# Optimization experiments

Hardware: AMD Instinct MI355X
Metric: run time of the kernel (lower is better)

Reference implementation:

```python
import jax, jax.numpy as jnp
import numpy as np

B, T, C = 2, 2048, 2048
HK, HV, DK, DV, KW = 16, 32, 128, 128, 4
KEY_DIM = HK * DK          # 2048
VAL_DIM = HV * DV          # 4096
QKV_DIM = 2 * KEY_DIM + VAL_DIM  # 8192
REPEAT = HV // HK
EPS = 1e-6


def setup_inputs() -> dict:
    key = jax.random.key(0)
    ks = jax.random.split(key, 12)
    s = 0.02
    return {
        "x": jax.random.normal(ks[0], (B, T, C), jnp.float32),
        "positions": jnp.arange(B * T, dtype=jnp.int64).reshape(B, T) % T,
        "W_qkv": jax.random.normal(ks[1], (QKV_DIM, C), jnp.float32) * s,
        "W_z": jax.random.normal(ks[2], (VAL_DIM, C), jnp.float32) * s,
        "W_b": jax.random.normal(ks[3], (HV, C), jnp.float32) * s,
        "W_a": jax.random.normal(ks[4], (HV, C), jnp.float32) * s,
        "conv_w": jax.random.normal(ks[5], (QKV_DIM, 1, KW), jnp.float32) * 0.3,
        "dt_bias": jnp.ones((HV,), jnp.float32),
        "A_log": jnp.log(jax.random.uniform(ks[6], (HV,), jnp.float32, 0.01, 16.0)),
        "norm_w": jnp.ones((DV,), jnp.float32),
        "W_out": jax.random.normal(ks[7], (C, VAL_DIM), jnp.float32) * s,
    }


def _forward(x, W_qkv, W_z, W_b, W_a, conv_w, dt_bias, A_log, norm_w, W_out):
    qkv = x @ W_qkv.T                                # [B,T,QKV_DIM]
    z = (x @ W_z.T).reshape(B, T, HV, DV)
    b = x @ W_b.T                                    # [B,T,HV]
    a = x @ W_a.T                                    # [B,T,HV]

    # depthwise causal conv1d (left pad KW-1), then SiLU
    qkv_c = jnp.transpose(qkv, (0, 2, 1))            # [B,QKV_DIM,T]
    qkv_c = jax.lax.conv_general_dilated(
        qkv_c, conv_w, window_strides=(1,), padding=[(KW - 1, 0)],
        dimension_numbers=("NCH", "OIH", "NCH"), feature_group_count=QKV_DIM)
    qkv = jax.nn.silu(jnp.transpose(qkv_c, (0, 2, 1)))

    q, k, v = jnp.split(qkv, [KEY_DIM, 2 * KEY_DIM], axis=-1)
    q = q.reshape(B, T, HK, DK)
    k = k.reshape(B, T, HK, DK)
    v = v.reshape(B, T, HV, DV)
    q = q / jnp.maximum(jnp.linalg.norm(q, axis=-1, keepdims=True), 1e-12)
    k = k / jnp.maximum(jnp.linalg.norm(k, axis=-1, keepdims=True), 1e-12)
    if REPEAT > 1:
        q = jnp.repeat(q, REPEAT, axis=2)            # [B,T,HV,DK]
        k = jnp.repeat(k, REPEAT, axis=2)

    beta = jax.nn.sigmoid(b)                         # [B,T,HV]
    g = -jnp.exp(A_log) * jax.nn.softplus(a + dt_bias)  # [B,T,HV]

    # gated delta-rule recurrence over time (lax.scan, time-major)
    def step(state, inp):
        g_t, beta_t, k_t, v_t, q_t = inp             # [B,HV], [B,HV], [B,HV,DK], [B,HV,DV], [B,HV,DK]
        state = jnp.exp(g_t)[..., None, None] * state \
            + beta_t[..., None, None] * (k_t[..., :, None] * v_t[..., None, :])
        out_t = jnp.einsum("bhk,bhkv->bhv", q_t, state)
        return state, out_t

    tm = lambda u: jnp.moveaxis(u, 1, 0)
    state0 = jnp.zeros((B, HV, DK, DV), x.dtype)
    _, out = jax.lax.scan(step, state0, (tm(g), tm(beta), tm(k), tm(v), tm(q)))
    out = jnp.moveaxis(out, 0, 1)                    # [B,T,HV,DV]

    # gated RMSNorm per head: RMSNorm(out) * silu(z)
    o = out.astype(jnp.float32)
    o = o * jax.lax.rsqrt(jnp.mean(o * o, axis=-1, keepdims=True) + EPS)
    o = (norm_w * o) * jax.nn.silu(z.astype(jnp.float32))
    o = o.astype(x.dtype).reshape(B, T, VAL_DIM)
    return o @ W_out.T                               # [B,T,C]


def reference(x, positions, W_qkv, W_z, W_b, W_a, conv_w, dt_bias, A_log, norm_w, W_out):
    del positions  # unused by the module's math
    return _forward(x, W_qkv, W_z, W_b, W_a, conv_w, dt_bias, A_log, norm_w, W_out)
```

## Files before the change

kernel.cpp:

```cpp
#include <hip/hip_runtime.h>

typedef unsigned short u16;
typedef unsigned int u32;
typedef __attribute__((ext_vector_type(8))) short short8;
typedef __attribute__((ext_vector_type(8))) _Float16 half8;
typedef __attribute__((ext_vector_type(4))) float f32x4;

#define NB 2
#define NT 2048
#define NC 2048
#define NHV 32
#define VALD 4096
#define NBT 4096
#define CL 64
#define NCH (NT / CL)

#define GL16(gp, lp) __builtin_amdgcn_global_load_lds( \
    (const __attribute__((address_space(1))) unsigned int*)(gp), \
    (__attribute__((address_space(3))) unsigned int*)(lp), 16, 0, 0)

static __device__ __forceinline__ float bf2f(u16 u) {
  union { u32 u; float f; } x; x.u = ((u32)u) << 16; return x.f;
}
static __device__ __forceinline__ u16 f2bf(float f) {
  union { float f; u32 u; } x; x.f = f;
  u32 r = x.u + 0x7fffu + ((x.u >> 16) & 1u);
  return (u16)(r >> 16);
}
static __device__ __forceinline__ u16 f2h(float f) {
  union { _Float16 h; u16 u; } c; c.h = (_Float16)f; return c.u;
}
static __device__ __forceinline__ float h2f(u16 u) {
  union { u16 u; _Float16 h; } c; c.u = u; return (float)c.h;
}
static __device__ __forceinline__ float sigm(float x) { return 1.0f / (1.0f + __expf(-x)); }
static __device__ __forceinline__ int ldsoff(int row, int c8) {
  return row * 48 + ((c8 ^ ((row >> 2) & 3)) << 3);
}

__global__ void k_sentinel(float* out) { out[0] = 1.0e6f; }

__global__ __launch_bounds__(256) void k_cvtx(const float* __restrict__ in, u16* __restrict__ hi,
                                              u16* __restrict__ lo, u16* __restrict__ h16, int n4) {
  int i = blockIdx.x * 256 + threadIdx.x;
  if (i >= n4) return;
  float4 v = ((const float4*)in)[i];
  ushort4 h, l, p;
  h.x = f2bf(v.x); l.x = f2bf(v.x - bf2f(h.x)); p.x = f2h(v.x);
  h.y = f2bf(v.y); l.y = f2bf(v.y - bf2f(h.y)); p.y = f2h(v.y);
  h.z = f2bf(v.z); l.z = f2bf(v.z - bf2f(h.z)); p.z = f2h(v.z);
  h.w = f2bf(v.w); l.w = f2bf(v.w - bf2f(h.w)); p.w = f2h(v.w);
  ((ushort4*)hi)[i] = h;
  ((ushort4*)lo)[i] = l;
  ((ushort4*)h16)[i] = p;
}

__global__ __launch_bounds__(256) void k_cvt16(const float* __restrict__ in, u16* __restrict__ out, int n4) {
  int i = blockIdx.x * 256 + threadIdx.x;
  if (i >= n4) return;
  float4 v = ((const float4*)in)[i];
  ushort4 o;
  o.x = f2h(v.x); o.y = f2h(v.y); o.z = f2h(v.z); o.w = f2h(v.w);
  ((ushort4*)out)[i] = o;
}

__global__ __launch_bounds__(256) void k_wba(const float* __restrict__ Wb, const float* __restrict__ Wa,
                                             u16* __restrict__ hi, u16* __restrict__ lo) {
  int i = blockIdx.x * 256 + threadIdx.x;
  int r = i >> 11, c = i & 2047;
  float v = 0.f;
  if (r < 32) v = Wb[r * 2048 + c];
  else if (r < 64) v = Wa[(r - 32) * 2048 + c];
  u16 h = f2bf(v);
  hi[i] = h;
  lo[i] = f2bf(v - bf2f(h));
}

__global__ __launch_bounds__(256) void k_gemm_bf3(const u16* __restrict__ Ahg, const u16* __restrict__ Alg,
                                                  const u16* __restrict__ Bhg, const u16* __restrict__ Blg,
                                                  float* __restrict__ C0, int M, int N, int K) {
  __shared__ __align__(16) u16 As_h[128 * 48];
  __shared__ __align__(16) u16 As_l[128 * 48];
  __shared__ __align__(16) u16 Bs_h[128 * 48];
  __shared__ __align__(16) u16 Bs_l[128 * 48];
  const int tid = threadIdx.x;
  const int lane = tid & 63, wave = tid >> 6;
  const int wr = wave >> 1, wc = wave & 1;
  const int l15 = lane & 15, l16 = lane >> 4;
  const int kc = blockIdx.x;
  const int Kc = K >> 2;
  const int kbase = kc * Kc;
  const int row0 = blockIdx.y * 128, col0 = 0;
  float* Cp = C0 + (size_t)kc * M * N;
  const int sr = tid >> 1, sk = (tid & 1) * 16;
  const int c0 = sk >> 3;
  const int w0 = ldsoff(sr, c0), w1 = ldsoff(sr, c0 + 1);
  f32x4 acc[4][4] = {};
  for (int k0 = kbase; k0 < kbase + Kc; k0 += 32) {
    const size_t aoff = (size_t)(row0 + sr) * K + k0 + sk;
    const size_t boff = (size_t)(col0 + sr) * K + k0 + sk;
    *(short8*)&As_h[w0] = *(const short8*)&Ahg[aoff];
    *(short8*)&As_h[w1] = *(const short8*)&Ahg[aoff + 8];
    *(short8*)&As_l[w0] = *(const short8*)&Alg[aoff];
    *(short8*)&As_l[w1] = *(const short8*)&Alg[aoff + 8];
    *(short8*)&Bs_h[w0] = *(const short8*)&Bhg[boff];
    *(short8*)&Bs_h[w1] = *(const short8*)&Bhg[boff + 8];
    *(short8*)&Bs_l[w0] = *(const short8*)&Blg[boff];
    *(short8*)&Bs_l[w1] = *(const short8*)&Blg[boff + 8];
    __syncthreads();
    short8 ah[4], al[4], bh[4], bl[4];
#pragma unroll
    for (int mi = 0; mi < 4; ++mi) {
      int off = ldsoff(wr * 64 + mi * 16 + l15, l16);
      ah[mi] = *(short8*)&As_h[off];
      al[mi] = *(short8*)&As_l[off];
    }
#pragma unroll
    for (int ni = 0; ni < 4; ++ni) {
      int off = ldsoff(wc * 64 + ni * 16 + l15, l16);
      bh[ni] = *(short8*)&Bs_h[off];
      bl[ni] = *(short8*)&Bs_l[off];
    }
#pragma unroll
    for (int mi = 0; mi < 4; ++mi)
#pragma unroll
      for (int ni = 0; ni < 4; ++ni) {
        acc[mi][ni] = __builtin_amdgcn_mfma_f32_16x16x32_bf16(ah[mi], bh[ni], acc[mi][ni], 0, 0, 0);
        acc[mi][ni] = __builtin_amdgcn_mfma_f32_16x16x32_bf16(al[mi], bh[ni], acc[mi][ni], 0, 0, 0);
        acc[mi][ni] = __builtin_amdgcn_mfma_f32_16x16x32_bf16(ah[mi], bl[ni], acc[mi][ni], 0, 0, 0);
      }
    __syncthreads();
  }
#pragma unroll
  for (int mi = 0; mi < 4; ++mi)
#pragma unroll
    for (int ni = 0; ni < 4; ++ni) {
      int rr = row0 + wr * 64 + mi * 16 + l16 * 4;
      int cc = col0 + wc * 64 + ni * 16 + l15;
#pragma unroll
      for (int i = 0; i < 4; ++i)
        Cp[(size_t)(rr + i) * N + cc] = acc[mi][ni][i];
    }
}

template <int MODE>
__global__ __launch_bounds__(256) void k_gemm16(const u16* __restrict__ Ag, const u16* __restrict__ Bg,
                                                void* __restrict__ C0, void* __restrict__ C1,
                                                int M, int N, int K,
                                                const u16* __restrict__ e0, const float* __restrict__ e1,
                                                const float* __restrict__ e2) {
  __shared__ __align__(16) u16 As[2 * 128 * 64];
  __shared__ __align__(16) u16 Bs[2 * 128 * 64];
  const int tid = threadIdx.x;
  const int lane = tid & 63, wave = tid >> 6;
  const int wr = wave >> 1, wc = wave & 1;
  const int l15 = lane & 15, l16 = lane >> 4;
  const int nbx = N >> 7;
  const int chunk = (int)gridDim.x >> 3;
  const int reg = (int)blockIdx.x & 7;
  const int t0i = (int)blockIdx.x >> 3;
  const int SC = (nbx < 16) ? nbx : 16;
  const int SR = chunk / SC;
  const int regc = nbx / SC;
  const int row0 = ((reg / regc) * SR + t0i / SC) * 128;
  const int col0 = ((reg % regc) * SC + t0i % SC) * 128;
  u32 gA[4], gB[4], lofs[4];
#pragma unroll
  for (int i = 0; i < 4; ++i) {
    int o = wave * 2048 + i * 512 + lane * 8;
    int row = o >> 6;
    int cg = ((lane & 7) ^ (row & 7)) * 8;
    gA[i] = (u32)(row0 + row) * (u32)K + cg;
    gB[i] = (u32)(col0 + row) * (u32)K + cg;
    lofs[i] = (u32)(wave * 2048 + i * 512);
  }
  f32x4 acc[4][4] = {};
  const int NTILE = K >> 6;
#pragma unroll
  for (int i = 0; i < 4; ++i) {
    GL16(Ag + gA[i], &As[lofs[i]]);
    GL16(Bg + gB[i], &Bs[lofs[i]]);
  }
  for (int t = 0; t < NTILE; ++t) {
    const u32 cb = (u32)(t & 1) * 8192;
    __syncthreads();
    if (t + 1 < NTILE) {
      const u32 nb = cb ^ 8192;
      const int kn = (t + 1) << 6;
#pragma unroll
      for (int i = 0; i < 4; ++i) {
        GL16(Ag + gA[i] + kn, &As[nb + lofs[i]]);
        GL16(Bg + gB[i] + kn, &Bs[nb + lofs[i]]);
      }
    }
#pragma unroll
    for (int kk = 0; kk < 2; ++kk) {
      half8 a[4], b[4];
#pragma unroll
      for (int mi = 0; mi < 4; ++mi) {
        int row = wr * 64 + mi * 16 + l15;
        a[mi] = *(half8*)&As[cb + row * 64 + (((kk * 4 + l16) ^ (l15 & 7)) << 3)];
      }
#pragma unroll
      for (int ni = 0; ni < 4; ++ni) {
        int row = wc * 64 + ni * 16 + l15;
        b[ni] = *(half8*)&Bs[cb + row * 64 + (((kk * 4 + l16) ^ (l15 & 7)) << 3)];
      }
#pragma unroll
      for (int mi = 0; mi < 4; ++mi)
#pragma unroll
        for (int ni = 0; ni < 4; ++ni)
          acc[mi][ni] = __builtin_amdgcn_mfma_f32_16x16x32_f16(a[mi], b[ni], acc[mi][ni], 0, 0, 0);
    }
  }
  u16* Cs = nullptr;
  int cbase = col0;
  if constexpr (MODE == 3) {
    Cs = (col0 < 4096) ? (u16*)C0 : (u16*)C1;
    cbase = col0 & 4095;
  }
#pragma unroll
  for (int mi = 0; mi < 4; ++mi) {
#pragma unroll
    for (int ni = 0; ni < 4; ++ni) {
      int rr = row0 + wr * 64 + mi * 16 + l16 * 4;
      int cc = col0 + wc * 64 + ni * 16 + l15;
#pragma unroll
      for (int i = 0; i < 4; ++i) {
        float v = acc[mi][ni][i];
        if constexpr (MODE == 0) {
          ((float*)C0)[(size_t)(rr + i) * N + cc] = v;
        } else if constexpr (MODE == 1) {
          ((u16*)C0)[(size_t)(rr + i) * N + cc] = f2h(v);
        } else if constexpr (MODE == 2) {
          size_t idx = (size_t)(rr + i) * N + cc;
          float zs = v * sigm(v);
          float o = h2f(e0[idx]) * e1[(size_t)(rr + i) * 32 + (cc >> 7)] * e2[cc & 127] * zs;
          ((u16*)C0)[idx] = f2h(o);
        } else {
          int c2 = cbase + wc * 64 + ni * 16 + l15;
          Cs[(size_t)(rr + i) * 4096 + c2] = f2h(v);
        }
      }
    }
  }
}

__global__ __launch_bounds__(256) void k_bg(const float* __restrict__ ba, const float* __restrict__ dt_bias,
                                            const float* __restrict__ A_log, float* __restrict__ beta_t,
                                            float* __restrict__ g_t) {
  int i = blockIdx.x * 256 + threadIdx.x;
  int bt = i >> 5, h = i & 31;
  const size_t P = (size_t)4096 * 128;
  float bv = ba[(size_t)bt * 128 + h] + ba[P + (size_t)bt * 128 + h] +
             ba[2 * P + (size_t)bt * 128 + h] + ba[3 * P + (size_t)bt * 128 + h];
  float av = ba[(size_t)bt * 128 + 32 + h] + ba[P + (size_t)bt * 128 + 32 + h] +
             ba[2 * P + (size_t)bt * 128 + 32 + h] + ba[3 * P + (size_t)bt * 128 + 32 + h];
  beta_t[h * 4096 + bt] = sigm(bv);
  float xx = av + dt_bias[h];
  float sp = (xx > 20.f) ? xx : log1pf(__expf(xx));
  g_t[h * 4096 + bt] = -__expf(A_log[h]) * sp;
}

__global__ __launch_bounds__(256) void k_convqk(const u16* __restrict__ qkraw, const float* __restrict__ cw,
                                                u16* __restrict__ qkn) {
  __shared__ float sval[4096];
  __shared__ float snrm[32];
  const int tid = threadIdx.x;
  const int bt = blockIdx.x;
  const int b = bt >> 11, t = bt & 2047;
  for (int i = 0; i < 16; ++i) {
    int c = i * 256 + tid;
    float acc = 0.f;
#pragma unroll
    for (int j = 0; j < 4; ++j) {
      int ts = t - 3 + j;
      if (ts >= 0) acc += cw[c * 4 + j] * h2f(qkraw[(size_t)(b * 2048 + ts) * 4096 + c]);
    }
    sval[c] = acc * sigm(acc);
  }
  __syncthreads();
  {
    int gidx = tid >> 3, s = tid & 7;
    float ss = 0.f;
#pragma unroll
    for (int i2 = 0; i2 < 16; ++i2) { float v = sval[gidx * 128 + s * 16 + i2]; ss += v * v; }
    ss += __shfl_xor(ss, 1); ss += __shfl_xor(ss, 2); ss += __shfl_xor(ss, 4);
    if (s == 0) snrm[gidx] = 1.0f / fmaxf(sqrtf(ss), 1e-12f);
  }
  __syncthreads();
  for (int i = 0; i < 16; ++i) {
    int c = i * 256 + tid;
    qkn[(size_t)bt * 4096 + c] = f2h(sval[c] * snrm[c >> 7]);
  }
}

__global__ __launch_bounds__(512, 4) void k_scanc(const u16* __restrict__ qk16, const u16* __restrict__ v16,
                                                  const float* __restrict__ cw,
                                                  const float* __restrict__ beta_t, const float* __restrict__ g_t,
                                                  u16* __restrict__ outr) {
  __shared__ __align__(16) u16 Qs[64][136], Ks[64][136];
  __shared__ __align__(16) u16 Vs[32][72];
  __shared__ __align__(16) u16 SIs[64][72];
  __shared__ __align__(16) u16 SH[2][32][132];
  __shared__ u16 rv16[67][36];
  __shared__ float garr[2][64], barr[2][64], warr[2][64], earr[2][64];
  __shared__ float sdt[2];

  const int tid = threadIdx.x;
  const int lane = tid & 63, wv = tid >> 6;
  const int l15 = lane & 15, l16 = lane >> 4;
  const int dq = blockIdx.x & 3, h = (blockIdx.x >> 2) & 31, b = blockIdx.x >> 7;
  const int bT = b * 2048;
  const int hk = h >> 1;
  const int dvl = tid & 31;
  const int vch = h * 128 + dq * 32;
  const float4 cwv = *(const float4*)&cw[(4096 + vch + dvl) * 4];
  const int mblk = wv & 3, nh = wv >> 2;
  const int m0 = mblk * 16;
  const int sr = tid >> 3, d0 = (tid & 7) * 16;
  const int r0v = tid >> 5;

  for (int i = tid; i < 2 * 32 * 132; i += 512) ((u16*)SH)[i] = 0;
  f32x4 st[2] = {};

  short8 pq[2], pk[2];
  u16 pv[5];
  float pgv, pbv;
  auto LOADQK = [&](int t0) {
    const size_t base = (size_t)(bT + t0 + sr) * 4096 + hk * 128 + d0;
    pq[0] = *(const short8*)&qk16[base];        pq[1] = *(const short8*)&qk16[base + 8];
    pk[0] = *(const short8*)&qk16[base + 2048]; pk[1] = *(const short8*)&qk16[base + 2056];
  };
  auto LOADV = [&](int t0) {
#pragma unroll
    for (int i = 0; i < 5; ++i) {
      int r = r0v + i * 16;
      int tr = t0 - 3 + r;
      pv[i] = (r < 67 && tr >= 0) ? v16[(size_t)(bT + tr) * 4096 + vch + dvl] : (u16)0;
    }
  };
  auto CUMSUM = [&](float gv, float bv, int buf) {
    float cum = gv;
#pragma unroll
    for (int off = 1; off < 64; off <<= 1) {
      float o = __shfl_up(cum, off);
      if (lane >= off) cum += o;
    }
    float tot = __shfl(cum, 63);
    garr[buf][lane] = cum;
    earr[buf][lane] = __expf(cum);
    warr[buf][lane] = __expf(tot - cum) * bv;
    barr[buf][lane] = bv;
    if (lane == 0) sdt[buf] = __expf(tot);
  };

  LOADQK(0);
  LOADV(0);
  if (wv == 0) {
    float gv = g_t[h * 4096 + bT + lane];
    float bv = beta_t[h * 4096 + bT + lane];
    CUMSUM(gv, bv, 0);
  }

  for (int ch = 0; ch < NCH; ++ch) {
    const int t0 = ch * CL;
    const int p = ch & 1;
    *(short8*)&Qs[sr][d0] = pq[0]; *(short8*)&Qs[sr][d0 + 8] = pq[1];
    *(short8*)&Ks[sr][d0] = pk[0]; *(short8*)&Ks[sr][d0 + 8] = pk[1];
#pragma unroll
    for (int i = 0; i < 5; ++i) {
      int r = r0v + i * 16;
      if (r < 67) rv16[r][dvl] = pv[i];
    }
    __syncthreads();
    if (ch + 1 < NCH) {
      LOADQK(t0 + CL);
      LOADV(t0 + CL);
      if (wv == 0) {
        pgv = g_t[h * 4096 + bT + t0 + CL + lane];
        pbv = beta_t[h * 4096 + bT + t0 + CL + lane];
      }
    }
    {
      int tl = tid >> 5;
#pragma unroll
      for (int rr = 0; rr < 4; ++rr) {
        int t = rr * 16 + tl;
        float a = cwv.x * h2f(rv16[t][dvl]) + cwv.y * h2f(rv16[t + 1][dvl]) +
                  cwv.z * h2f(rv16[t + 2][dvl]) + cwv.w * h2f(rv16[t + 3][dvl]);
        a = a * sigm(a);
        Vs[dvl][t] = f2h(a);
      }
    }
    half8 a[4];
#pragma unroll
    for (int kk = 0; kk < 4; ++kk) a[kk] = *(half8*)&Qs[m0 + l15][l16 * 8 + kk * 32];
#pragma unroll
    for (int j = 0; j < 2; ++j) {
      int n = nh * 2 + j;
      f32x4 a4 = {};
#pragma unroll
      for (int kk = 0; kk < 4; ++kk) {
        half8 b8 = *(half8*)&Ks[n * 16 + l15][l16 * 8 + kk * 32];
        a4 = __builtin_amdgcn_mfma_f32_16x16x32_f16(a[kk], b8, a4, 0, 0, 0);
      }
      int col = n * 16 + l15;
      float gc = garr[p][col], bc = barr[p][col];
#pragma unroll
      for (int i = 0; i < 4; ++i) {
        int row = m0 + l16 * 4 + i;
        float cval = (col <= row) ? __expf(garr[p][row] - gc) * bc * a4[i] : 0.f;
        SIs[row][col] = f2h(cval);
      }
    }
    __syncthreads();
    f32x4 ao = {};
#pragma unroll
    for (int kk = 0; kk < 4; ++kk) {
      half8 s8 = *(half8*)&SH[p][nh * 16 + l15][l16 * 8 + kk * 32];
      ao = __builtin_amdgcn_mfma_f32_16x16x32_f16(a[kk], s8, ao, 0, 0, 0);
    }
#pragma unroll
    for (int i = 0; i < 4; ++i) ao[i] *= earr[p][m0 + l16 * 4 + i];
#pragma unroll
    for (int kk = 0; kk < 2; ++kk) {
      half8 asi = *(half8*)&SIs[m0 + l15][l16 * 8 + kk * 32];
      half8 bv8 = *(half8*)&Vs[nh * 16 + l15][l16 * 8 + kk * 32];
      ao = __builtin_amdgcn_mfma_f32_16x16x32_f16(asi, bv8, ao, 0, 0, 0);
    }
#pragma unroll
    for (int i = 0; i < 4; ++i)
      outr[(size_t)(bT + t0 + m0 + l16 * 4 + i) * 4096 + vch + nh * 16 + l15] = f2h(ao[i]);
    const float sd = sdt[p];
#pragma unroll
    for (int m = 0; m < 2; ++m)
#pragma unroll
      for (int i = 0; i < 4; ++i) st[m][i] *= sd;
#pragma unroll
    for (int kk = 0; kk < 2; ++kk) {
      half8 bw;
      {
        int dk = wv * 16 + l15;
#pragma unroll
        for (int e = 0; e < 8; ++e) {
          int s = l16 * 8 + e + kk * 32;
          bw[e] = (_Float16)(h2f(Ks[s][dk]) * warr[p][s]);
        }
      }
#pragma unroll
      for (int m = 0; m < 2; ++m) {
        half8 av = *(half8*)&Vs[m * 16 + l15][l16 * 8 + kk * 32];
        st[m] = __builtin_amdgcn_mfma_f32_16x16x32_f16(av, bw, st[m], 0, 0, 0);
      }
    }
#pragma unroll
    for (int m = 0; m < 2; ++m)
#pragma unroll
      for (int i = 0; i < 4; ++i)
        SH[p ^ 1][m * 16 + l16 * 4 + i][wv * 16 + l15] = f2h(st[m][i]);
    if (wv == 0 && ch + 1 < NCH) CUMSUM(pgv, pbv, p ^ 1);
    __syncthreads();
  }
}

__global__ __launch_bounds__(256) void k_rms(const u16* __restrict__ outr, float* __restrict__ rms) {
  int pair = blockIdx.x * 4 + (threadIdx.x >> 6);
  int lane = threadIdx.x & 63;
  u32 pv = *(const u32*)&outr[(size_t)pair * 128 + lane * 2];
  float v0 = h2f((u16)pv), v1 = h2f((u16)(pv >> 16));
  float ss = v0 * v0 + v1 * v1;
#pragma unroll
  for (int m = 1; m < 64; m <<= 1) ss += __shfl_xor(ss, m);
  if (lane == 0) rms[pair] = rsqrtf(ss * (1.0f / 128.0f) + 1e-6f);
}

extern "C" void kernel_launch(void* const* d_in, const int* in_sizes, int n_in,
                              void* d_out, int out_size, void* d_ws, size_t ws_size,
                              hipStream_t stream) {
  const float* x = (const float*)d_in[0];
  const float* W_qkv = (const float*)d_in[2];
  const float* W_z = (const float*)d_in[3];
  const float* W_b = (const float*)d_in[4];
  const float* W_a = (const float*)d_in[5];
  const float* conv_w = (const float*)d_in[6];
  const float* dt_bias = (const float*)d_in[7];
  const float* A_log = (const float*)d_in[8];
  const float* norm_w = (const float*)d_in[9];
  const float* W_out = (const float*)d_in[10];
  float* out = (float*)d_out;

  const size_t MB = 1ull << 20;
  const size_t need = 192 * MB + 3 * (size_t)NBT * 32 * 4;
  if (ws_size < need) {
    k_sentinel<<<1, 1, 0, stream>>>(out);
    return;
  }
  char* ws = (char*)d_ws;
  u16* xh = (u16*)ws;
  u16* xl = (u16*)(ws + 16 * MB);
  u16* xh16 = (u16*)(ws + 32 * MB);
  u16* wz16 = (u16*)(ws + 48 * MB);
  u16* qkB16 = (u16*)(ws + 64 * MB);
  u16* wout16 = (u16*)(ws + 64 * MB);
  u16* qkA16 = (u16*)(ws + 96 * MB);
  u16* om16 = (u16*)(ws + 96 * MB);
  u16* wsh16 = (u16*)(ws + 128 * MB);
  u16* outr16 = (u16*)(ws + 128 * MB);
  u16* v16 = (u16*)(ws + 160 * MB);
  u16* wbah = (u16*)(ws + 160 * MB);
  u16* wbal = (u16*)(ws + 160 * MB + 512 * 1024);
  float* babuf4 = (float*)(ws + 161 * MB);
  float* beta_t = (float*)(ws + 192 * MB);
  float* g_t = beta_t + (size_t)NBT * 32;
  float* rmsb = g_t + (size_t)NBT * 32;

  const int N4X = NBT * NC / 4;
  k_cvtx<<<N4X / 256, 256, 0, stream>>>(x, xh, xl, xh16, N4X);
  k_cvt16<<<2 * N4X / 256, 256, 0, stream>>>(W_qkv, wsh16, 2 * N4X);
  k_cvt16<<<N4X / 256, 256, 0, stream>>>(W_z, wz16, N4X);
  k_wba<<<128 * NC / 256, 256, 0, stream>>>(W_b, W_a, wbah, wbal);
  k_gemm_bf3<<<dim3(4, NBT / 128), 256, 0, stream>>>(xh, xl, wbah, wbal, babuf4, NBT, 128, NC);
  k_bg<<<NBT * 32 / 256, 256, 0, stream>>>(babuf4, dt_bias, A_log, beta_t, g_t);

  k_gemm16<3><<<(NBT / 128) * (8192 / 128), 256, 0, stream>>>(xh16, wsh16, qkA16, v16,
                                                              NBT, 8192, NC, nullptr, nullptr, nullptr);
  k_convqk<<<NBT, 256, 0, stream>>>(qkA16, conv_w, qkB16);

  k_scanc<<<256, 512, 0, stream>>>(qkB16, v16, conv_w, beta_t, g_t, outr16);
  k_rms<<<NBT * NHV / 4, 256, 0, stream>>>(outr16, rmsb);

  k_gemm16<2><<<(NBT / 128) * (VALD / 128), 256, 0, stream>>>(xh16, wz16, om16, nullptr, NBT, VALD, NC,
                                                              outr16, rmsb, norm_w);

  k_cvt16<<<N4X / 256, 256, 0, stream>>>(W_out, wout16, N4X);
  k_gemm16<0><<<(NBT / 128) * (NC / 128), 256, 0, stream>>>(om16, wout16, out, nullptr, NBT, NC, VALD,
                                                            nullptr, nullptr, nullptr);
}
```

Baseline: 571.7 us.

## Load Q fragments directly into registers and cut LDS for higher occupancy

The chunked scan kernel no longer stages Q in shared memory. Each wave loads its Q MFMA fragments straight from global memory into registers, double-buffered through a prefetch array. The earr table is dropped and exp(cumsum) is recomputed inline, and the rv16 padding shrinks, reducing LDS use. With that, launch bounds are raised from 4 to 6 blocks per CU to target higher occupancy. The trade-off is more register pressure from the extra half8 prefetch buffers, possible spills under the tighter bound, and redundant Q global loads across the waves that share a row block.

```diff
diff --git a/kernel.cpp b/kernel.cpp
--- a/kernel.cpp
+++ b/kernel.cpp
@@ -295,16 +295,16 @@
   }
 }
 
-__global__ __launch_bounds__(512, 4) void k_scanc(const u16* __restrict__ qk16, const u16* __restrict__ v16,
+__global__ __launch_bounds__(512, 6) void k_scanc(const u16* __restrict__ qk16, const u16* __restrict__ v16,
                                                   const float* __restrict__ cw,
                                                   const float* __restrict__ beta_t, const float* __restrict__ g_t,
                                                   u16* __restrict__ outr) {
-  __shared__ __align__(16) u16 Qs[64][136], Ks[64][136];
+  __shared__ __align__(16) u16 Ks[64][136];
   __shared__ __align__(16) u16 Vs[32][72];
   __shared__ __align__(16) u16 SIs[64][72];
   __shared__ __align__(16) u16 SH[2][32][132];
-  __shared__ u16 rv16[67][36];
-  __shared__ float garr[2][64], barr[2][64], warr[2][64], earr[2][64];
+  __shared__ u16 rv16[67][33];
+  __shared__ float garr[2][64], barr[2][64], warr[2][64];
   __shared__ float sdt[2];
 
   const int tid = threadIdx.x;
@@ -324,13 +324,19 @@
   for (int i = tid; i < 2 * 32 * 132; i += 512) ((u16*)SH)[i] = 0;
   f32x4 st[2] = {};
 
-  short8 pq[2], pk[2];
+  short8 pk[2];
+  half8 aq[4], pa[4];
   u16 pv[5];
   float pgv, pbv;
-  auto LOADQK = [&](int t0) {
-    const size_t base = (size_t)(bT + t0 + sr) * 4096 + hk * 128 + d0;
-    pq[0] = *(const short8*)&qk16[base];        pq[1] = *(const short8*)&qk16[base + 8];
-    pk[0] = *(const short8*)&qk16[base + 2048]; pk[1] = *(const short8*)&qk16[base + 2056];
+  auto LOADK = [&](int t0) {
+    const size_t base = (size_t)(bT + t0 + sr) * 4096 + 2048 + hk * 128 + d0;
+    pk[0] = *(const short8*)&qk16[base];
+    pk[1] = *(const short8*)&qk16[base + 8];
+  };
+  auto LOADQ = [&](int t0, half8* dst) {
+    const size_t qrow = (size_t)(bT + t0 + m0 + l15) * 4096 + hk * 128 + l16 * 8;
+#pragma unroll
+    for (int kk = 0; kk < 4; ++kk) dst[kk] = *(const half8*)&qk16[qrow + kk * 32];
   };
   auto LOADV = [&](int t0) {
 #pragma unroll
@@ -349,13 +355,13 @@
     }
     float tot = __shfl(cum, 63);
     garr[buf][lane] = cum;
-    earr[buf][lane] = __expf(cum);
     warr[buf][lane] = __expf(tot - cum) * bv;
     barr[buf][lane] = bv;
     if (lane == 0) sdt[buf] = __expf(tot);
   };
 
-  LOADQK(0);
+  LOADK(0);
+  LOADQ(0, aq);
   LOADV(0);
   if (wv == 0) {
     float gv = g_t[h * 4096 + bT + lane];
@@ -366,7 +372,6 @@
   for (int ch = 0; ch < NCH; ++ch) {
     const int t0 = ch * CL;
     const int p = ch & 1;
-    *(short8*)&Qs[sr][d0] = pq[0]; *(short8*)&Qs[sr][d0 + 8] = pq[1];
     *(short8*)&Ks[sr][d0] = pk[0]; *(short8*)&Ks[sr][d0 + 8] = pk[1];
 #pragma unroll
     for (int i = 0; i < 5; ++i) {
@@ -375,7 +380,8 @@
     }
     __syncthreads();
     if (ch + 1 < NCH) {
-      LOADQK(t0 + CL);
+      LOADK(t0 + CL);
+      LOADQ(t0 + CL, pa);
       LOADV(t0 + CL);
       if (wv == 0) {
         pgv = g_t[h * 4096 + bT + t0 + CL + lane];
@@ -393,9 +399,6 @@
         Vs[dvl][t] = f2h(a);
       }
     }
-    half8 a[4];
-#pragma unroll
-    for (int kk = 0; kk < 4; ++kk) a[kk] = *(half8*)&Qs[m0 + l15][l16 * 8 + kk * 32];
 #pragma unroll
     for (int j = 0; j < 2; ++j) {
       int n = nh * 2 + j;
@@ -403,7 +406,7 @@
 #pragma unroll
       for (int kk = 0; kk < 4; ++kk) {
         half8 b8 = *(half8*)&Ks[n * 16 + l15][l16 * 8 + kk * 32];
-        a4 = __builtin_amdgcn_mfma_f32_16x16x32_f16(a[kk], b8, a4, 0, 0, 0);
+        a4 = __builtin_amdgcn_mfma_f32_16x16x32_f16(aq[kk], b8, a4, 0, 0, 0);
       }
       int col = n * 16 + l15;
       float gc = garr[p][col], bc = barr[p][col];
@@ -419,10 +422,10 @@
 #pragma unroll
     for (int kk = 0; kk < 4; ++kk) {
       half8 s8 = *(half8*)&SH[p][nh * 16 + l15][l16 * 8 + kk * 32];
-      ao = __builtin_amdgcn_mfma_f32_16x16x32_f16(a[kk], s8, ao, 0, 0, 0);
-    }
-#pragma unroll
-    for (int i = 0; i < 4; ++i) ao[i] *= earr[p][m0 + l16 * 4 + i];
+      ao = __builtin_amdgcn_mfma_f32_16x16x32_f16(aq[kk], s8, ao, 0, 0, 0);
+    }
+#pragma unroll
+    for (int i = 0; i < 4; ++i) ao[i] *= __expf(garr[p][m0 + l16 * 4 + i]);
 #pragma unroll
     for (int kk = 0; kk < 2; ++kk) {
       half8 asi = *(half8*)&SIs[m0 + l15][l16 * 8 + kk * 32];
@@ -460,6 +463,8 @@
       for (int i = 0; i < 4; ++i)
         SH[p ^ 1][m * 16 + l16 * 4 + i][wv * 16 + l15] = f2h(st[m][i]);
     if (wv == 0 && ch + 1 < NCH) CUMSUM(pgv, pbv, p ^ 1);
+#pragma unroll
+    for (int kk = 0; kk < 4; ++kk) aq[kk] = pa[kk];
     __syncthreads();
   }
 }
```

Result: slower. 749.1 us (+31.0%).
